# Kernel optimization log

Hardware: AMD Instinct MI355X
Metric: run time of the kernel (lower is better)

The kernel has to match this reference:

```python
import jax, jax.numpy as jnp
import numpy as np

EPS = 1.1920929e-07  # torch.finfo(float32).eps, default for F.rms_norm
HQ, HKV = 16, 4
WIN = 256

def rmsnorm(x):
    return x * jax.lax.rsqrt(jnp.mean(x * x, axis=-1, keepdims=True) + EPS)

def setup_inputs() -> dict:
    key = jax.random.key(0)
    ks = jax.random.split(key, 5)
    B, T, C = 2, 2048, 2048
    Dh = C // HQ
    s = 0.02
    x = jax.random.normal(ks[0], (B, T, C), jnp.float32)
    Wq = jax.random.normal(ks[1], (C, HQ * Dh), jnp.float32) * s
    Wk = jax.random.normal(ks[2], (C, HKV * Dh), jnp.float32) * s
    Wv = jax.random.normal(ks[3], (C, HKV * Dh), jnp.float32) * s
    Wo = jax.random.normal(ks[4], (C, C), jnp.float32) * s
    return {"x": x, "Wq": Wq, "Wk": Wk, "Wv": Wv, "Wo": Wo}

def reference(x, Wq, Wk, Wv, Wo):
    B, T, C = x.shape
    Dh = C // HQ
    g = HQ // HKV
    # projections (Linear bias=False); weights stored [in,out]
    Q = (x @ Wq).reshape(B, T, HQ, Dh).transpose(0, 2, 1, 3)   # [B,Hq,T,Dh]
    V = (x @ Wv).reshape(B, T, HKV, Dh).transpose(0, 2, 1, 3)  # [B,Hkv,T,Dh]
    _K_unused = x @ Wk  # source computes c_k(x) but then overwrites K = norm(V)
    Q = rmsnorm(Q)
    K = rmsnorm(V)  # faithful to source bug: K = norm(V)
    Q = Q.reshape(B, HKV, g, T, Dh)
    scores = jnp.einsum('bhgtd,bhsd->bhgts', Q, K)  # no 1/sqrt(Dh) scale, as in source
    i = jnp.arange(T)[:, None]
    j = jnp.arange(T)[None, :]
    mask = (j > i) & (j <= i - WIN)
    scores = jnp.where(mask, -jnp.inf, scores)
    p = jax.nn.softmax(scores, axis=-1)
    y = jnp.einsum('bhgts,bhsd->bhgtd', p, V)
    y = y.reshape(B, HQ, T, Dh).transpose(0, 2, 1, 3).reshape(B, T, C)
    return rmsnorm(y @ Wo)
```

## Files before the change

kernel.cpp:

```cpp
#include <hip/hip_runtime.h>
#include <math.h>

#define BB   2
#define TT   2048
#define CC   2048
#define HQ_  16
#define HKV_ 4
#define DH   128
#define MM   (BB * TT)
#define KVC  (HKV_ * DH)
#define QVN  (CC + KVC)

typedef __attribute__((ext_vector_type(8)))  _Float16 f16x8;
typedef __attribute__((ext_vector_type(4)))  float    f32x4;

__device__ __forceinline__ unsigned short f2h(float x) {
    _Float16 h = (_Float16)x;
    return __builtin_bit_cast(unsigned short, h);
}
__device__ __forceinline__ float h2f(unsigned short u) {
    return (float)__builtin_bit_cast(_Float16, u);
}
__device__ __forceinline__ void gll16(const void* g, void* l) {
    __builtin_amdgcn_global_load_lds(
        (const __attribute__((address_space(1))) unsigned int*)g,
        (__attribute__((address_space(3))) unsigned int*)l, 16, 0, 0);
}
__device__ __forceinline__ int xcd_swizzle(int lid, int nwg) {
    const int xcd = lid & 7, rank = lid >> 3;
    const int q8 = nwg >> 3, r8 = nwg & 7;
    return (xcd < r8 ? xcd * (q8 + 1) : r8 * (q8 + 1) + (xcd - r8) * q8) + rank;
}

__device__ __forceinline__ void tcast_tile(const float* __restrict__ W,
                                           unsigned short* __restrict__ WT,
                                           int Kd, int Nd, int n0, int k0,
                                           float Ls[32][33]) {
    const int i = threadIdx.x;
    {
        const int kr = i >> 3, n4 = (i & 7) * 4;
        float4 v = *(const float4*)&W[(size_t)(k0 + kr) * Nd + n0 + n4];
        Ls[kr][n4 + 0] = v.x; Ls[kr][n4 + 1] = v.y;
        Ls[kr][n4 + 2] = v.z; Ls[kr][n4 + 3] = v.w;
    }
    __syncthreads();
    {
        const int nr = i >> 3, k4 = (i & 7) * 4;
        uint2 o;
        o.x = (unsigned)f2h(Ls[k4 + 0][nr]) | ((unsigned)f2h(Ls[k4 + 1][nr]) << 16);
        o.y = (unsigned)f2h(Ls[k4 + 2][nr]) | ((unsigned)f2h(Ls[k4 + 3][nr]) << 16);
        *(uint2*)&WT[(size_t)(n0 + nr) * Kd + k0 + k4] = o;
    }
}

__global__ __launch_bounds__(256)
void prep(const float* __restrict__ x,  unsigned short* __restrict__ xb,
          const float* __restrict__ Wq, const float* __restrict__ Wv,
          const float* __restrict__ Wo, unsigned short* __restrict__ WqvT,
          unsigned short* __restrict__ WoT) {
    __shared__ float Ls[32][33];
    const int bid = blockIdx.x;
    if (bid < 2048) {
        const int n8 = MM * CC / 8;
        int i = bid * 256 + threadIdx.x;
        for (; i < n8; i += 2048 * 256) {
            const float4 a = ((const float4*)x)[i * 2 + 0];
            const float4 b = ((const float4*)x)[i * 2 + 1];
            uint4 o;
            o.x = (unsigned)f2h(a.x) | ((unsigned)f2h(a.y) << 16);
            o.y = (unsigned)f2h(a.z) | ((unsigned)f2h(a.w) << 16);
            o.z = (unsigned)f2h(b.x) | ((unsigned)f2h(b.y) << 16);
            o.w = (unsigned)f2h(b.z) | ((unsigned)f2h(b.w) << 16);
            ((uint4*)xb)[i] = o;
        }
    } else if (bid < 2048 + 4096) {
        const int t = bid - 2048;
        tcast_tile(Wq, WqvT, CC, CC, (t & 63) * 32, (t >> 6) * 32, Ls);
    } else if (bid < 2048 + 4096 + 1024) {
        const int t = bid - (2048 + 4096);
        tcast_tile(Wv, WqvT + (size_t)CC * CC, CC, KVC, (t & 15) * 32, (t >> 4) * 32, Ls);
    } else {
        const int t = bid - (2048 + 4096 + 1024);
        tcast_tile(Wo, WoT, CC, CC, (t & 63) * 32, (t >> 6) * 32, Ls);
    }
}

template<int F16OUT>
__global__ __launch_bounds__(256)
void gemm_bt(const unsigned short* __restrict__ A, const unsigned short* __restrict__ Bt,
             void* __restrict__ Cout, int M, int N, int K) {
    __shared__ __align__(16) unsigned short As[128 * 64];
    __shared__ __align__(16) unsigned short Bs[128 * 64];
    const int tid  = threadIdx.x;
    const int lane = tid & 63, wid = tid >> 6;
    const int g = lane >> 4, l15 = lane & 15;
    const int nwg  = gridDim.x * gridDim.y;
    const int tile = xcd_swizzle(blockIdx.y * gridDim.x + blockIdx.x, nwg);
    const int bm = (tile / gridDim.x) * 128, bn = (tile % gridDim.x) * 128;
    const int wr = (wid >> 1) * 64, wc = (wid & 1) * 64;

    f32x4 acc[4][4] = {};

    for (int kt = 0; kt < K; kt += 64) {
        __syncthreads();
#pragma unroll
        for (int r = 0; r < 4; ++r) {
            const int q = r * 256 + tid;
            const int row = q >> 3, c = q & 7, sc = c ^ (row & 7);
            gll16(A + (size_t)(bm + row) * K + kt + sc * 8, As + q * 8);
        }
#pragma unroll
        for (int r = 0; r < 4; ++r) {
            const int q = r * 256 + tid;
            const int row = q >> 3, c = q & 7, sc = c ^ (row & 7);
            gll16(Bt + (size_t)(bn + row) * K + kt + sc * 8, Bs + q * 8);
        }
        __syncthreads();

#pragma unroll
        for (int kk = 0; kk < 2; ++kk) {
            f16x8 af[4], bfr[4];
#pragma unroll
            for (int m = 0; m < 4; ++m) {
                const int row = wr + m * 16 + l15;
                const int ch = (kk * 4 + g) ^ (row & 7);
                af[m] = *(const f16x8*)&As[row * 64 + ch * 8];
            }
#pragma unroll
            for (int n = 0; n < 4; ++n) {
                const int row = wc + n * 16 + l15;
                const int ch = (kk * 4 + g) ^ (row & 7);
                bfr[n] = *(const f16x8*)&Bs[row * 64 + ch * 8];
            }
#pragma unroll
            for (int m = 0; m < 4; ++m)
#pragma unroll
                for (int n = 0; n < 4; ++n)
                    acc[m][n] = __builtin_amdgcn_mfma_f32_16x16x32_f16(
                        af[m], bfr[n], acc[m][n], 0, 0, 0);
        }
    }

#pragma unroll
    for (int m = 0; m < 4; ++m)
#pragma unroll
        for (int n = 0; n < 4; ++n)
#pragma unroll
            for (int r = 0; r < 4; ++r) {
                const int row = bm + wr + m * 16 + g * 4 + r;
                const int col = bn + wc + n * 16 + l15;
                const float v = acc[m][n][r];
                if (F16OUT)
                    ((unsigned short*)Cout)[(size_t)row * N + col] = f2h(v);
                else
                    ((float*)Cout)[(size_t)row * N + col] = v;
            }
}

__global__ __launch_bounds__(256)
void kvprep(const unsigned short* __restrict__ Vg,
            unsigned short* __restrict__ Kb, unsigned short* __restrict__ Vt) {
    __shared__ unsigned short Ls[32][132];
    const int t0 = blockIdx.x * 32;
    const int bh = blockIdx.y;
    const int b = bh >> 2, hk = bh & 3;
    const int tid = threadIdx.x;

    const int tr = tid >> 3, c16 = (tid & 7) * 16;
    const unsigned short* src =
        Vg + (size_t)(b * TT + t0 + tr) * QVN + hk * DH + c16;
    const uint4 u0 = *(const uint4*)(src);
    const uint4 u1 = *(const uint4*)(src + 8);
    *(uint4*)&Ls[tr][c16]     = u0;
    *(uint4*)&Ls[tr][c16 + 8] = u1;

    float v[16];
    {
        const unsigned uu[8] = {u0.x, u0.y, u0.z, u0.w, u1.x, u1.y, u1.z, u1.w};
#pragma unroll
        for (int j = 0; j < 8; ++j) {
            v[2 * j]     = h2f((unsigned short)(uu[j] & 0xffff));
            v[2 * j + 1] = h2f((unsigned short)(uu[j] >> 16));
        }
    }
    float ss = 0.f;
#pragma unroll
    for (int j = 0; j < 16; ++j) ss += v[j] * v[j];
    ss += __shfl_xor(ss, 1);
    ss += __shfl_xor(ss, 2);
    ss += __shfl_xor(ss, 4);
    const float sc = rsqrtf(ss * (1.f / DH) + 1.1920929e-07f);

    {
        unsigned short* kd = Kb + (size_t)(b * TT + t0 + tr) * KVC + hk * DH + c16;
        unsigned oo[8];
#pragma unroll
        for (int j = 0; j < 8; ++j)
            oo[j] = (unsigned)f2h(v[2 * j] * sc) | ((unsigned)f2h(v[2 * j + 1] * sc) << 16);
        *(uint4*)(kd)     = make_uint4(oo[0], oo[1], oo[2], oo[3]);
        *(uint4*)(kd + 8) = make_uint4(oo[4], oo[5], oo[6], oo[7]);
    }
    __syncthreads();

    {
        const int dr = tid >> 1, t16 = (tid & 1) * 16;
        unsigned oo[8];
#pragma unroll
        for (int j = 0; j < 8; ++j)
            oo[j] = (unsigned)Ls[t16 + 2 * j][dr] | ((unsigned)Ls[t16 + 2 * j + 1][dr] << 16);
        unsigned short* dst = Vt + ((size_t)bh * DH + dr) * TT + t0 + t16;
        *(uint4*)(dst)     = make_uint4(oo[0], oo[1], oo[2], oo[3]);
        *(uint4*)(dst + 8) = make_uint4(oo[4], oo[5], oo[6], oo[7]);
    }
}

__global__ __launch_bounds__(256, 4)
void attn_mfma(const unsigned short* __restrict__ Qb, const unsigned short* __restrict__ Kb,
               const unsigned short* __restrict__ Vt, unsigned short* __restrict__ Yb) {
    __shared__ __align__(16) unsigned short Ks[2][32 * 128];
    __shared__ __align__(16) unsigned short Vs[2][128 * 32];
    __shared__ __align__(16) unsigned short Ps[4][16 * 32];

    const int tid  = threadIdx.x;
    const int lane = tid & 63, wid = tid >> 6;
    const int g = lane >> 4, l15 = lane & 15;
    const int q0 = blockIdx.x * 64;
    const int bh = blockIdx.y;
    const int b = bh >> 4, h = bh & 15, hk = h >> 2;

    const size_t kbase = (size_t)(b * TT) * KVC + hk * DH;
    const size_t vbase = (size_t)(b * HKV_ + hk) * DH * TT;

#define STAGE(buf, st)                                                         \
    do {                                                                       \
        _Pragma("unroll")                                                      \
        for (int r = 0; r < 2; ++r) {                                          \
            const int qq = r * 256 + tid;                                      \
            const int key = qq >> 4, c = qq & 15, sc = c ^ (key & 7);          \
            gll16(Kb + kbase + (size_t)((st) + key) * KVC + sc * 8,            \
                  &Ks[buf][qq * 8]);                                           \
        }                                                                      \
        _Pragma("unroll")                                                      \
        for (int r = 0; r < 2; ++r) {                                          \
            const int qq = r * 256 + tid;                                      \
            const int d = qq >> 2, c = qq & 3;                                 \
            const int sc = c ^ (d & 3) ^ ((d >> 2) & 3);                       \
            gll16(Vt + vbase + (size_t)d * TT + (st) + sc * 8,                 \
                  &Vs[buf][qq * 8]);                                           \
        }                                                                      \
    } while (0)

    STAGE(0, 0);

    f16x8 qf[4];
    {
        const unsigned short* qp =
            Qb + (size_t)(b * TT + q0 + wid * 16 + l15) * QVN + h * DH + g * 8;
#pragma unroll
        for (int kk = 0; kk < 4; ++kk) qf[kk] = *(const f16x8*)(qp + kk * 32);
    }
    {
        float ss = 0.f;
#pragma unroll
        for (int kk = 0; kk < 4; ++kk)
#pragma unroll
            for (int j = 0; j < 8; ++j) { const float v = (float)qf[kk][j]; ss += v * v; }
        ss += __shfl_xor(ss, 16);
        ss += __shfl_xor(ss, 32);
        const float qsc = rsqrtf(ss * (1.f / DH) + 1.1920929e-07f) * 1.4426950408889634f;
#pragma unroll
        for (int kk = 0; kk < 4; ++kk)
#pragma unroll
            for (int j = 0; j < 8; ++j)
                qf[kk][j] = (_Float16)((float)qf[kk][j] * qsc);
    }

    f16x8 ones_b;
    {
        const _Float16 v = (l15 == 0) ? (_Float16)1.0f : (_Float16)0.0f;
#pragma unroll
        for (int j = 0; j < 8; ++j) ones_b[j] = v;
    }

    float mr[4];
    f32x4 acc[9] = {};
#pragma unroll
    for (int r = 0; r < 4; ++r) mr[r] = -3.0e38f;

    unsigned short* pw = Ps[wid];

    asm volatile("s_waitcnt vmcnt(0)" ::: "memory");
    __builtin_amdgcn_s_barrier();

    const int NT = TT / 32;
    for (int t = 0; t < NT; ++t) {
        const int cur = t & 1;
        if (t + 1 < NT) STAGE(cur ^ 1, (t + 1) * 32);

        const unsigned short* ksp = Ks[cur];
        const unsigned short* vsp = Vs[cur];

        f32x4 s[2] = {};
        __builtin_amdgcn_s_setprio(1);
#pragma unroll
        for (int kk = 0; kk < 4; ++kk)
#pragma unroll
            for (int n = 0; n < 2; ++n) {
                const int key = n * 16 + l15;
                const int ch = (kk * 4 + g) ^ (key & 7);
                const f16x8 kf = *(const f16x8*)&ksp[key * 128 + ch * 8];
                s[n] = __builtin_amdgcn_mfma_f32_16x16x32_f16(qf[kk], kf, s[n], 0, 0, 0);
            }
        __builtin_amdgcn_s_setprio(0);

        float m0[4];
        bool need = false;
#pragma unroll
        for (int r = 0; r < 4; ++r) {
            m0[r] = fmaxf(s[0][r], s[1][r]);
            need = need || (m0[r] > mr[r] + 8.f);
        }
        if (__any(need)) {
            float scale[4];
#pragma unroll
            for (int r = 0; r < 4; ++r) {
                float mx = m0[r];
#pragma unroll
                for (int o = 8; o >= 1; o >>= 1) mx = fmaxf(mx, __shfl_xor(mx, o));
                const float mn = fmaxf(mr[r], mx);
                scale[r] = __builtin_amdgcn_exp2f(mr[r] - mn);
                mr[r] = mn;
            }
#pragma unroll
            for (int f = 0; f < 9; ++f) {
                acc[f][0] *= scale[0]; acc[f][1] *= scale[1];
                acc[f][2] *= scale[2]; acc[f][3] *= scale[3];
            }
        }

#pragma unroll
        for (int n = 0; n < 2; ++n) {
            const int colc = n * 2 + (l15 >> 3);
            const int cel  = l15 & 7;
#pragma unroll
            for (int r = 0; r < 4; ++r) {
                const float p = __builtin_amdgcn_exp2f(s[n][r] - mr[r]);
                const int row = g * 4 + r;
                const int ch = colc ^ (row & 3) ^ g;
                pw[row * 32 + ch * 8 + cel] = f2h(p);
            }
        }

        __builtin_amdgcn_s_setprio(1);
        {
            const int ch = g ^ (l15 & 3) ^ ((l15 >> 2) & 3);
            const f16x8 pa = *(const f16x8*)&pw[l15 * 32 + ch * 8];
#pragma unroll
            for (int f = 0; f < 8; ++f) {
                const int dr = f * 16 + l15;
                const int vch = g ^ (dr & 3) ^ ((dr >> 2) & 3);
                const f16x8 vf = *(const f16x8*)&vsp[dr * 32 + vch * 8];
                acc[f] = __builtin_amdgcn_mfma_f32_16x16x32_f16(pa, vf, acc[f], 0, 0, 0);
            }
            acc[8] = __builtin_amdgcn_mfma_f32_16x16x32_f16(pa, ones_b, acc[8], 0, 0, 0);
        }
        __builtin_amdgcn_s_setprio(0);

        asm volatile("s_waitcnt vmcnt(0)" ::: "memory");
        __builtin_amdgcn_s_barrier();
    }
#undef STAGE

    float inv[4];
#pragma unroll
    for (int r = 0; r < 4; ++r) {
        const float l = __shfl(acc[8][r], lane & 48);
        inv[r] = 1.f / l;
    }
#pragma unroll
    for (int f = 0; f < 8; ++f)
#pragma unroll
        for (int r = 0; r < 4; ++r) {
            const int t = q0 + wid * 16 + g * 4 + r;
            const int col = h * DH + f * 16 + l15;
            Yb[(size_t)(b * TT + t) * CC + col] = f2h(acc[f][r] * inv[r]);
        }
}

__global__ __launch_bounds__(256)
void rms2048_h(const unsigned short* __restrict__ in, float* __restrict__ out) {
    __shared__ float red[4];
    const int tid = threadIdx.x;
    const unsigned short* p = in + (size_t)blockIdx.x * CC + tid * 8;
    const uint4 u = *(const uint4*)p;
    float v[8];
    v[0] = h2f((unsigned short)(u.x & 0xffff)); v[1] = h2f((unsigned short)(u.x >> 16));
    v[2] = h2f((unsigned short)(u.y & 0xffff)); v[3] = h2f((unsigned short)(u.y >> 16));
    v[4] = h2f((unsigned short)(u.z & 0xffff)); v[5] = h2f((unsigned short)(u.z >> 16));
    v[6] = h2f((unsigned short)(u.w & 0xffff)); v[7] = h2f((unsigned short)(u.w >> 16));
    float ss = 0.f;
#pragma unroll
    for (int j = 0; j < 8; ++j) ss += v[j] * v[j];
#pragma unroll
    for (int o = 32; o >= 1; o >>= 1) ss += __shfl_xor(ss, o);
    if ((tid & 63) == 0) red[tid >> 6] = ss;
    __syncthreads();
    const float tot = red[0] + red[1] + red[2] + red[3];
    const float sc = rsqrtf(tot * (1.f / CC) + 1.1920929e-07f);
    float* q = out + (size_t)blockIdx.x * CC + tid * 8;
    *(float4*)&q[0] = make_float4(v[0] * sc, v[1] * sc, v[2] * sc, v[3] * sc);
    *(float4*)&q[4] = make_float4(v[4] * sc, v[5] * sc, v[6] * sc, v[7] * sc);
}

extern "C" void kernel_launch(void* const* d_in, const int* in_sizes, int n_in,
                              void* d_out, int out_size, void* d_ws, size_t ws_size,
                              hipStream_t stream) {
    const float* x  = (const float*)d_in[0];
    const float* Wq = (const float*)d_in[1];
    const float* Wv = (const float*)d_in[3];
    const float* Wo = (const float*)d_in[4];
    float* out = (float*)d_out;

    char* ws = (char*)d_ws;
    const size_t MB = 1024 * 1024;
    unsigned short* xb   = (unsigned short*)(ws);
    unsigned short* WqvT = (unsigned short*)(ws + 16 * MB);
    unsigned short* QVg  = (unsigned short*)(ws + 26 * MB);
    unsigned short* Kb   = (unsigned short*)(ws + 46 * MB);
    unsigned short* Vt   = (unsigned short*)(ws + 50 * MB);
    unsigned short* Yb   = (unsigned short*)(ws + 54 * MB);
    unsigned short* WoT  = (unsigned short*)(ws + 70 * MB);

    const unsigned short* Qb = QVg;
    const unsigned short* Vg = QVg + CC;

    const dim3 blk(256);

    prep<<<11264, blk, 0, stream>>>(x, xb, Wq, Wv, Wo, WqvT, WoT);

    gemm_bt<1><<<dim3(QVN / 128, MM / 128), blk, 0, stream>>>(xb, WqvT, QVg, MM, QVN, CC);

    kvprep<<<dim3(TT / 32, BB * HKV_), blk, 0, stream>>>(Vg, Kb, Vt);

    attn_mfma<<<dim3(TT / 64, BB * HQ_), blk, 0, stream>>>(Qb, Kb, Vt, Yb);

    gemm_bt<1><<<dim3(CC / 128, MM / 128), blk, 0, stream>>>(Yb, WoT, xb, MM, CC, CC);
    rms2048_h<<<MM, blk, 0, stream>>>(xb, out);
}
```

Measured before the change: 266.5 us.

## Switch attention to 32x32x16 MFMA with 2-wave blocks and register-resident P

```diff
diff --git a/kernel.cpp b/kernel.cpp
--- a/kernel.cpp
+++ b/kernel.cpp
@@ -13,6 +13,7 @@
 
 typedef __attribute__((ext_vector_type(8)))  _Float16 f16x8;
 typedef __attribute__((ext_vector_type(4)))  float    f32x4;
+typedef __attribute__((ext_vector_type(16))) float    f32x16;
 
 __device__ __forceinline__ unsigned short f2h(float x) {
     _Float16 h = (_Float16)x;
@@ -20,6 +21,9 @@
 }
 __device__ __forceinline__ float h2f(unsigned short u) {
     return (float)__builtin_bit_cast(_Float16, u);
+}
+__device__ __forceinline__ unsigned pk2(float a, float b) {
+    return (unsigned)f2h(a) | ((unsigned)f2h(b) << 16);
 }
 __device__ __forceinline__ void gll16(const void* g, void* l) {
     __builtin_amdgcn_global_load_lds(
@@ -67,10 +71,8 @@
             const float4 a = ((const float4*)x)[i * 2 + 0];
             const float4 b = ((const float4*)x)[i * 2 + 1];
             uint4 o;
-            o.x = (unsigned)f2h(a.x) | ((unsigned)f2h(a.y) << 16);
-            o.y = (unsigned)f2h(a.z) | ((unsigned)f2h(a.w) << 16);
-            o.z = (unsigned)f2h(b.x) | ((unsigned)f2h(b.y) << 16);
-            o.w = (unsigned)f2h(b.z) | ((unsigned)f2h(b.w) << 16);
+            o.x = pk2(a.x, a.y); o.y = pk2(a.z, a.w);
+            o.z = pk2(b.x, b.y); o.w = pk2(b.z, b.w);
             ((uint4*)xb)[i] = o;
         }
     } else if (bid < 2048 + 4096) {
@@ -196,7 +198,7 @@
         unsigned oo[8];
 #pragma unroll
         for (int j = 0; j < 8; ++j)
-            oo[j] = (unsigned)f2h(v[2 * j] * sc) | ((unsigned)f2h(v[2 * j + 1] * sc) << 16);
+            oo[j] = pk2(v[2 * j] * sc, v[2 * j + 1] * sc);
         *(uint4*)(kd)     = make_uint4(oo[0], oo[1], oo[2], oo[3]);
         *(uint4*)(kd + 8) = make_uint4(oo[4], oo[5], oo[6], oo[7]);
     }
@@ -214,16 +216,16 @@
     }
 }
 
-__global__ __launch_bounds__(256, 4)
+__global__ __launch_bounds__(128, 2)
 void attn_mfma(const unsigned short* __restrict__ Qb, const unsigned short* __restrict__ Kb,
                const unsigned short* __restrict__ Vt, unsigned short* __restrict__ Yb) {
     __shared__ __align__(16) unsigned short Ks[2][32 * 128];
     __shared__ __align__(16) unsigned short Vs[2][128 * 32];
-    __shared__ __align__(16) unsigned short Ps[4][16 * 32];
+    __shared__ float Lbc[2][32];
 
     const int tid  = threadIdx.x;
     const int lane = tid & 63, wid = tid >> 6;
-    const int g = lane >> 4, l15 = lane & 15;
+    const int l31 = lane & 31, g2 = lane >> 5;
     const int q0 = blockIdx.x * 64;
     const int bh = blockIdx.y;
     const int b = bh >> 4, h = bh & 15, hk = h >> 2;
@@ -234,15 +236,16 @@
 #define STAGE(buf, st)                                                         \
     do {                                                                       \
         _Pragma("unroll")                                                      \
-        for (int r = 0; r < 2; ++r) {                                          \
-            const int qq = r * 256 + tid;                                      \
-            const int key = qq >> 4, c = qq & 15, sc = c ^ (key & 7);          \
+        for (int r = 0; r < 4; ++r) {                                          \
+            const int qq = r * 128 + tid;                                      \
+            const int key = qq >> 4, c = qq & 15;                              \
+            const int sc = c ^ (key & 7) ^ (((key >> 3) & 1) << 3);            \
             gll16(Kb + kbase + (size_t)((st) + key) * KVC + sc * 8,            \
                   &Ks[buf][qq * 8]);                                           \
         }                                                                      \
         _Pragma("unroll")                                                      \
-        for (int r = 0; r < 2; ++r) {                                          \
-            const int qq = r * 256 + tid;                                      \
+        for (int r = 0; r < 4; ++r) {                                          \
+            const int qq = r * 128 + tid;                                      \
             const int d = qq >> 2, c = qq & 3;                                 \
             const int sc = c ^ (d & 3) ^ ((d >> 2) & 3);                       \
             gll16(Vt + vbase + (size_t)d * TT + (st) + sc * 8,                 \
@@ -252,42 +255,30 @@
 
     STAGE(0, 0);
 
-    f16x8 qf[4];
+    f16x8 qf[8];
     {
         const unsigned short* qp =
-            Qb + (size_t)(b * TT + q0 + wid * 16 + l15) * QVN + h * DH + g * 8;
-#pragma unroll
-        for (int kk = 0; kk < 4; ++kk) qf[kk] = *(const f16x8*)(qp + kk * 32);
+            Qb + (size_t)(b * TT + q0 + wid * 32 + l31) * QVN + h * DH + g2 * 8;
+#pragma unroll
+        for (int s = 0; s < 8; ++s) qf[s] = *(const f16x8*)(qp + s * 16);
     }
     {
         float ss = 0.f;
 #pragma unroll
-        for (int kk = 0; kk < 4; ++kk)
-#pragma unroll
-            for (int j = 0; j < 8; ++j) { const float v = (float)qf[kk][j]; ss += v * v; }
-        ss += __shfl_xor(ss, 16);
+        for (int s = 0; s < 8; ++s)
+#pragma unroll
+            for (int j = 0; j < 8; ++j) { const float v = (float)qf[s][j]; ss += v * v; }
         ss += __shfl_xor(ss, 32);
         const float qsc = rsqrtf(ss * (1.f / DH) + 1.1920929e-07f) * 1.4426950408889634f;
 #pragma unroll
-        for (int kk = 0; kk < 4; ++kk)
+        for (int s = 0; s < 8; ++s)
 #pragma unroll
             for (int j = 0; j < 8; ++j)
-                qf[kk][j] = (_Float16)((float)qf[kk][j] * qsc);
-    }
-
-    f16x8 ones_b;
-    {
-        const _Float16 v = (l15 == 0) ? (_Float16)1.0f : (_Float16)0.0f;
-#pragma unroll
-        for (int j = 0; j < 8; ++j) ones_b[j] = v;
-    }
-
-    float mr[4];
-    f32x4 acc[9] = {};
-#pragma unroll
-    for (int r = 0; r < 4; ++r) mr[r] = -3.0e38f;
-
-    unsigned short* pw = Ps[wid];
+                qf[s][j] = (_Float16)((float)qf[s][j] * qsc);
+    }
+
+    float mr = -3.0e38f, lr = 0.f;
+    f32x16 accO[4] = {};
 
     asm volatile("s_waitcnt vmcnt(0)" ::: "memory");
     __builtin_amdgcn_s_barrier();
@@ -300,69 +291,66 @@
         const unsigned short* ksp = Ks[cur];
         const unsigned short* vsp = Vs[cur];
 
-        f32x4 s[2] = {};
+        f32x16 sA = {};
         __builtin_amdgcn_s_setprio(1);
 #pragma unroll
-        for (int kk = 0; kk < 4; ++kk)
-#pragma unroll
-            for (int n = 0; n < 2; ++n) {
-                const int key = n * 16 + l15;
-                const int ch = (kk * 4 + g) ^ (key & 7);
-                const f16x8 kf = *(const f16x8*)&ksp[key * 128 + ch * 8];
-                s[n] = __builtin_amdgcn_mfma_f32_16x16x32_f16(qf[kk], kf, s[n], 0, 0, 0);
+        for (int s = 0; s < 8; ++s) {
+            const int kch = (2 * s + g2) ^ (l31 & 7) ^ (((l31 >> 3) & 1) << 3);
+            const f16x8 kf = *(const f16x8*)&ksp[l31 * 128 + kch * 8];
+            sA = __builtin_amdgcn_mfma_f32_32x32x16_f16(kf, qf[s], sA, 0, 0, 0);
+        }
+        __builtin_amdgcn_s_setprio(0);
+
+        float m0 = sA[0];
+#pragma unroll
+        for (int r = 1; r < 16; ++r) m0 = fmaxf(m0, sA[r]);
+        const float pairm = fmaxf(m0, __shfl_xor(m0, 32));
+        const bool need = pairm > mr + 8.f;
+        if (__any(need)) {
+            const float mn = fmaxf(mr, pairm);
+            const float sc = __builtin_amdgcn_exp2f(mr - mn);
+            mr = mn;
+            lr *= sc;
+            Lbc[wid][l31] = sc;
+#pragma unroll
+            for (int r = 0; r < 16; ++r) {
+                const int qr = (r & 3) + 8 * (r >> 2) + 4 * g2;
+                const float scr = Lbc[wid][qr];
+                accO[0][r] *= scr; accO[1][r] *= scr;
+                accO[2][r] *= scr; accO[3][r] *= scr;
             }
-        __builtin_amdgcn_s_setprio(0);
-
-        float m0[4];
-        bool need = false;
-#pragma unroll
-        for (int r = 0; r < 4; ++r) {
-            m0[r] = fmaxf(s[0][r], s[1][r]);
-            need = need || (m0[r] > mr[r] + 8.f);
-        }
-        if (__any(need)) {
-            float scale[4];
-#pragma unroll
-            for (int r = 0; r < 4; ++r) {
-                float mx = m0[r];
-#pragma unroll
-                for (int o = 8; o >= 1; o >>= 1) mx = fmaxf(mx, __shfl_xor(mx, o));
-                const float mn = fmaxf(mr[r], mx);
-                scale[r] = __builtin_amdgcn_exp2f(mr[r] - mn);
-                mr[r] = mn;
+        }
+
+        float p[16];
+        float s16 = 0.f;
+#pragma unroll
+        for (int r = 0; r < 16; ++r) {
+            p[r] = __builtin_amdgcn_exp2f(sA[r] - mr);
+            s16 += p[r];
+        }
+        lr += s16 + __shfl_xor(s16, 32);
+
+        __builtin_amdgcn_s_setprio(1);
+#pragma unroll
+        for (int ks = 0; ks < 2; ++ks) {
+            const unsigned w0 = pk2(p[8 * ks + 0], p[8 * ks + 1]);
+            const unsigned w1 = pk2(p[8 * ks + 2], p[8 * ks + 3]);
+            const unsigned w2 = pk2(p[8 * ks + 4], p[8 * ks + 5]);
+            const unsigned w3 = pk2(p[8 * ks + 6], p[8 * ks + 7]);
+            const unsigned sw0 = __shfl_xor(w0, 32);
+            const unsigned sw1 = __shfl_xor(w1, 32);
+            const unsigned sw2 = __shfl_xor(w2, 32);
+            const unsigned sw3 = __shfl_xor(w3, 32);
+            const uint4 uw = (g2 == 0) ? make_uint4(w0, w1, sw0, sw1)
+                                       : make_uint4(sw2, sw3, w2, w3);
+            const f16x8 pa = __builtin_bit_cast(f16x8, uw);
+#pragma unroll
+            for (int db = 0; db < 4; ++db) {
+                const int dr = db * 32 + l31;
+                const int vch = (2 * ks + g2) ^ (dr & 3) ^ ((dr >> 2) & 3);
+                const f16x8 vf = *(const f16x8*)&vsp[dr * 32 + vch * 8];
+                accO[db] = __builtin_amdgcn_mfma_f32_32x32x16_f16(pa, vf, accO[db], 0, 0, 0);
             }
-#pragma unroll
-            for (int f = 0; f < 9; ++f) {
-                acc[f][0] *= scale[0]; acc[f][1] *= scale[1];
-                acc[f][2] *= scale[2]; acc[f][3] *= scale[3];
-            }
-        }
-
-#pragma unroll
-        for (int n = 0; n < 2; ++n) {
-            const int colc = n * 2 + (l15 >> 3);
-            const int cel  = l15 & 7;
-#pragma unroll
-            for (int r = 0; r < 4; ++r) {
-                const float p = __builtin_amdgcn_exp2f(s[n][r] - mr[r]);
-                const int row = g * 4 + r;
-                const int ch = colc ^ (row & 3) ^ g;
-                pw[row * 32 + ch * 8 + cel] = f2h(p);
-            }
-        }
-
-        __builtin_amdgcn_s_setprio(1);
-        {
-            const int ch = g ^ (l15 & 3) ^ ((l15 >> 2) & 3);
-            const f16x8 pa = *(const f16x8*)&pw[l15 * 32 + ch * 8];
-#pragma unroll
-            for (int f = 0; f < 8; ++f) {
-                const int dr = f * 16 + l15;
-                const int vch = g ^ (dr & 3) ^ ((dr >> 2) & 3);
-                const f16x8 vf = *(const f16x8*)&vsp[dr * 32 + vch * 8];
-                acc[f] = __builtin_amdgcn_mfma_f32_16x16x32_f16(pa, vf, acc[f], 0, 0, 0);
-            }
-            acc[8] = __builtin_amdgcn_mfma_f32_16x16x32_f16(pa, ones_b, acc[8], 0, 0, 0);
         }
         __builtin_amdgcn_s_setprio(0);
 
@@ -371,20 +359,18 @@
     }
 #undef STAGE
 
-    float inv[4];
-#pragma unroll
-    for (int r = 0; r < 4; ++r) {
-        const float l = __shfl(acc[8][r], lane & 48);
-        inv[r] = 1.f / l;
-    }
-#pragma unroll
-    for (int f = 0; f < 8; ++f)
-#pragma unroll
-        for (int r = 0; r < 4; ++r) {
-            const int t = q0 + wid * 16 + g * 4 + r;
-            const int col = h * DH + f * 16 + l15;
-            Yb[(size_t)(b * TT + t) * CC + col] = f2h(acc[f][r] * inv[r]);
-        }
+    Lbc[wid][l31] = 1.f / lr;
+#pragma unroll
+    for (int r = 0; r < 16; ++r) {
+        const int qr = (r & 3) + 8 * (r >> 2) + 4 * g2;
+        const float inv = Lbc[wid][qr];
+        const int trow = q0 + wid * 32 + qr;
+#pragma unroll
+        for (int db = 0; db < 4; ++db) {
+            const int col = h * DH + db * 32 + l31;
+            Yb[(size_t)(b * TT + trow) * CC + col] = f2h(accO[db][r] * inv);
+        }
+    }
 }
 
 __global__ __launch_bounds__(256)
@@ -442,7 +428,7 @@
 
     kvprep<<<dim3(TT / 32, BB * HKV_), blk, 0, stream>>>(Vg, Kb, Vt);
 
-    attn_mfma<<<dim3(TT / 64, BB * HQ_), blk, 0, stream>>>(Qb, Kb, Vt, Yb);
+    attn_mfma<<<dim3(TT / 64, BB * HQ_), dim3(128), 0, stream>>>(Qb, Kb, Vt, Yb);
 
     gemm_bt<1><<<dim3(CC / 128, MM / 128), blk, 0, stream>>>(Yb, WoT, xb, MM, CC, CC);
     rms2048_h<<<MM, blk, 0, stream>>>(xb, out);
```

After: 244.4 us. -8.3%, faster.
